# Kernel optimization log

Hardware: AMD Instinct MI355X
Metric: run time of the kernel (lower is better)

Reference implementation:

```python
import jax, jax.numpy as jnp
import numpy as np

B, L, H, N, CIN, COUT, U = 32, 12, 12, 2048, 2, 1, 64
K3 = 3  # num_matrices = n_supports * max_diffusion_step + 1 = 1*2 + 1


def setup_inputs() -> dict:
    rng = np.random.default_rng(0)
    # random sparse-ish symmetric adjacency -> scaled laplacian support (lambda_max ~= 2)
    A = rng.random((N, N), dtype=np.float32)
    A = np.maximum(A, A.T)
    A = A * (A > 0.995)
    d = A.sum(axis=1)
    dis = 1.0 / np.sqrt(np.maximum(d, 1e-6))
    Lap = np.eye(N, dtype=np.float32) - (dis[:, None] * A) * dis[None, :]
    support = (Lap - np.eye(N, dtype=np.float32)).astype(np.float32)  # 2/lmax*L - I with lmax=2

    key = jax.random.key(0)
    ks = jax.random.split(key, 6)

    def w(k, shape, fan):
        return jax.random.normal(k, shape, jnp.float32) / np.float32(np.sqrt(fan))

    Cg_e = (CIN + U) * K3   # 198
    Cg_d = (COUT + U) * K3  # 195
    return {
        "history_data": jax.random.normal(ks[0], (B, L, N, CIN), jnp.float32),
        "support": jnp.asarray(support),
        "enc_Wg": w(ks[1], (Cg_e, 2 * U), Cg_e),
        "enc_bg": jnp.ones((2 * U,), jnp.float32),  # gate bias starts at 1.0 (original repo)
        "enc_Wc": w(ks[2], (Cg_e, U), Cg_e),
        "enc_bc": jnp.zeros((U,), jnp.float32),
        "dec_Wg": w(ks[3], (Cg_d, 2 * U), Cg_d),
        "dec_bg": jnp.ones((2 * U,), jnp.float32),
        "dec_Wc": w(ks[4], (Cg_d, U), Cg_d),
        "dec_bc": jnp.zeros((U,), jnp.float32),
        "Wp": w(ks[5], (U, COUT), U),
        "bp": jnp.zeros((COUT,), jnp.float32),
    }


def _gconv(support, x, W, b):
    # x: [B, N, C]; Chebyshev diffusion T0=x, T1=Sx, T2=2S(Sx)-x, stacked feature-major
    x1 = jnp.einsum('mn,bnc->bmc', support, x)
    x2 = 2.0 * jnp.einsum('mn,bnc->bmc', support, x1) - x
    xs = jnp.stack([x, x1, x2], axis=-1)  # [B, N, C, 3]
    b_, n_, c_, k_ = xs.shape
    y = xs.reshape(b_ * n_, c_ * k_) @ W + b
    return y.reshape(b_, n_, -1)


def _cell(support, x, h, Wg, bg, Wc, bc):
    # DCGRU cell: x [B,N,in], h [B,N,U]
    cat = jnp.concatenate([x, h], axis=-1)
    ru = jax.nn.sigmoid(_gconv(support, cat, Wg, bg))
    r, u = jnp.split(ru, 2, axis=-1)
    c = jnp.tanh(_gconv(support, jnp.concatenate([x, r * h], axis=-1), Wc, bc))
    return u * h + (1.0 - u) * c


def reference(history_data, support, enc_Wg, enc_bg, enc_Wc, enc_bc,
              dec_Wg, dec_bg, dec_Wc, dec_bc, Wp, bp):
    hist = jnp.transpose(history_data, (1, 0, 2, 3))  # [L, B, N, CIN]
    h0 = jnp.zeros((B, N, U), history_data.dtype)

    def enc_step(h, xt):
        return _cell(support, xt, h, enc_Wg, enc_bg, enc_Wc, enc_bc), None

    h_enc, _ = jax.lax.scan(enc_step, h0, hist)

    go = jnp.zeros((B, N, COUT), history_data.dtype)

    def dec_step(carry, _):
        h, xin = carry
        h = _cell(support, xin, h, dec_Wg, dec_bg, dec_Wc, dec_bc)
        out = (h.reshape(-1, U) @ Wp + bp).reshape(B, N, COUT)
        return (h, out), out

    _, outs = jax.lax.scan(dec_step, (h_enc, go), None, length=H)  # [H, B, N, COUT]
    return jnp.transpose(outs, (1, 0, 2, 3))  # [B, H, N, COUT]
```

## Files before the change

kernel.cpp:

```cpp
#include <hip/hip_runtime.h>
#include <math.h>

#define NN 2048
#define BB 32
#define LL 12
#define HHH 12
#define UU 64
#define STR 68
#define SLAB (BB*STR)
#define SEGS 8
#define SEGW (SLAB/SEGS)
#define MR (NN*BB)
#define CSR_CAP 262144
#define PACK_HALF 28672

typedef short bfrag __attribute__((ext_vector_type(8)));
typedef float ffrag __attribute__((ext_vector_type(4)));

__device__ __forceinline__ unsigned packsf(float x) {
  unsigned u = __float_as_uint(x);
  unsigned hb = (u + 0x7FFFu + ((u >> 16) & 1u)) & 0xFFFF0000u;
  float rem = x - __uint_as_float(hb);
  unsigned lb = __float_as_uint(rem) >> 16;
  return hb | lb;
}
__device__ __forceinline__ float recsf(unsigned u) {
  return __uint_as_float(u & 0xFFFF0000u) + __uint_as_float(u << 16);
}
__device__ __forceinline__ float sigm(float x) { return 1.0f / (1.0f + __expf(-x)); }
__device__ __forceinline__ float tanhfast(float x) {
  float e = __expf(2.0f * x);
  return 1.0f - 2.0f / (e + 1.0f);
}

__global__ __launch_bounds__(256) void k_row_count(const float* __restrict__ S, int* __restrict__ cnt) {
  int m = blockIdx.x;
  const float* row = S + (size_t)m * NN;
  int c = 0;
  for (int i = threadIdx.x; i < NN; i += 256) c += (row[i] != 0.0f);
  __shared__ int sm[4];
  for (int off = 32; off; off >>= 1) c += __shfl_down(c, off, 64);
  if ((threadIdx.x & 63) == 0) sm[threadIdx.x >> 6] = c;
  __syncthreads();
  if (threadIdx.x == 0) cnt[m] = sm[0] + sm[1] + sm[2] + sm[3];
}

__global__ __launch_bounds__(256) void k_scan(const int* __restrict__ cnt, int* __restrict__ rp) {
  __shared__ int tot[256];
  int t = threadIdx.x;
  int base = t * 8;
  int v[8]; int s = 0;
  #pragma unroll
  for (int k = 0; k < 8; ++k) { v[k] = cnt[base + k]; s += v[k]; }
  tot[t] = s;
  __syncthreads();
  for (int off = 1; off < 256; off <<= 1) {
    int add = (t >= off) ? tot[t - off] : 0;
    __syncthreads();
    tot[t] += add;
    __syncthreads();
  }
  int run = (t == 0) ? 0 : tot[t - 1];
  #pragma unroll
  for (int k = 0; k < 8; ++k) { rp[base + k] = run; run += v[k]; }
  if (t == 255) rp[NN] = run;
}

__global__ __launch_bounds__(256) void k_fill(const float* __restrict__ S, const int* __restrict__ rp,
                                              int* __restrict__ cols, float* __restrict__ vals) {
  int m = blockIdx.x;
  const float* row = S + (size_t)m * NN;
  __shared__ int wsum[4];
  __shared__ int chunkbase;
  if (threadIdx.x == 0) chunkbase = rp[m];
  __syncthreads();
  int lane = threadIdx.x & 63, w = threadIdx.x >> 6;
  for (int ch = 0; ch < NN / 256; ++ch) {
    int i = ch * 256 + threadIdx.x;
    float val = row[i];
    bool p = (val != 0.0f);
    unsigned long long mask = __ballot(p);
    int rank = __popcll(mask & ((1ull << lane) - 1ull));
    if (lane == 0) wsum[w] = __popcll(mask);
    __syncthreads();
    int off = 0;
    for (int q = 0; q < w; ++q) off += wsum[q];
    if (p) { int k = chunkbase + off + rank; cols[k] = i; vals[k] = val; }
    __syncthreads();
    if (threadIdx.x == 0) chunkbase += wsum[0] + wsum[1] + wsum[2] + wsum[3];
    __syncthreads();
  }
}

__global__ __launch_bounds__(256) void k_pack(const float* __restrict__ Wsrc, unsigned short* __restrict__ dst,
                                              int CIN_, int NO) {
  int idx = blockIdx.x * 256 + threadIdx.x;
  int nh_count = NO >> 6;
  int tot = nh_count * 7 * 4 * 64 * 8;
  if (idx >= tot) return;
  int j = idx & 7;
  int r1 = idx >> 3;  int lane = r1 & 63;
  int r2 = r1 >> 6;   int nf = r2 & 3;
  int r3 = r2 >> 2;   int ks = r3 % 7; int nh = r3 / 7;
  int grp = lane >> 4, l15 = lane & 15;
  int col = nh*64 + nf*16 + l15;
  float wv = 0.0f;
  int kb = -1, c = 0;
  if (ks < 6) {
    kb = ks >> 1;
    c = CIN_ + (ks & 1)*32 + grp*8 + j;
  } else {
    int q = grp*8 + j;
    if (q < 3*CIN_) { kb = q / CIN_; c = q % CIN_; }
  }
  if (kb >= 0) {
    float w0 = Wsrc[((size_t)c*3 + 0)*NO + col];
    float w1 = Wsrc[((size_t)c*3 + 1)*NO + col];
    float w2 = Wsrc[((size_t)c*3 + 2)*NO + col];
    wv = (kb == 0) ? (w0 - w2) : ((kb == 1) ? w1 : 2.0f*w2);
  }
  unsigned pw = packsf(wv);
  size_t basehi = ((size_t)nh*PACK_HALF) + ((((size_t)ks*4 + nf)*2 + 0)*64 + lane)*8 + j;
  size_t baselo = ((size_t)nh*PACK_HALF) + ((((size_t)ks*4 + nf)*2 + 1)*64 + lane)*8 + j;
  dst[basehi] = (unsigned short)(pw >> 16);
  dst[baselo] = (unsigned short)(pw & 0xFFFFu);
}

__global__ __launch_bounds__(256) void k_packt(const float* __restrict__ src, unsigned* __restrict__ dst, int n) {
  int i = blockIdx.x * 256 + threadIdx.x;
  if (i < n) dst[i] = packsf(src[i]);
}

template<int SRC>
__global__ __launch_bounds__(256, 4) void k_hop(
    const int* __restrict__ rp, const int* __restrict__ cols, const float* __restrict__ vals,
    const unsigned* __restrict__ src, const unsigned* __restrict__ xP,
    const unsigned* __restrict__ hP, unsigned* __restrict__ Y, int t) {
  __shared__ int   scol[64];
  __shared__ float sval[64];
  int orig = blockIdx.x;
  int swz = (orig & 7) * 2048 + (orig >> 3);
  int seg = swz >> 11;
  int node = swz & 2047;
  int j0 = rp[node], j1 = rp[node + 1];
  int tid = threadIdx.x;
  int w0 = seg * SEGW + tid;
  bool a1 = tid < (SEGW - 256);
  int w1 = w0 + 256;
  float acc0 = 0.f, acc1 = 0.f;

  const unsigned *bp0, *bp1;
  unsigned st0, st1;
  bool z0 = false, z1 = false;
  if constexpr (SRC == 0) {
    bp0 = src + w0; st0 = SLAB;
    bp1 = src + (a1 ? w1 : w0); st1 = SLAB; z1 = !a1;
  } else {
    auto mk = [&](int wq, const unsigned*& bp, unsigned& st, bool& zz) {
      int b = wq / STR, c = wq - b * STR;
      if (c < 64) { bp = hP + (size_t)b * UU + c; st = BB * UU; }
      else if (SRC == 1 && c < 66) { bp = xP + ((size_t)(b * LL + t)) * NN * 2 + (c - 64); st = 2; }
      else if (SRC == 2 && c == 64) { bp = xP + b; st = BB; }
      else { bp = hP; st = 0; zz = true; }
    };
    mk(w0, bp0, st0, z0);
    if (a1) mk(w1, bp1, st1, z1);
    else { bp1 = hP; st1 = 0; z1 = true; }
  }

  for (int base = j0; base < j1; base += 64) {
    int cnt = min(64, j1 - base);
    if (tid < cnt) { scol[tid] = cols[base + tid]; sval[tid] = vals[base + tid]; }
    __syncthreads();
    int jj = 0;
    for (; jj + 8 <= cnt; jj += 8) {
      unsigned u0[8], u1[8];
      float sv[8];
      #pragma unroll
      for (int q = 0; q < 8; ++q) {
        unsigned n = (unsigned)scol[jj + q];
        sv[q] = sval[jj + q];
        u0[q] = bp0[(size_t)(n * st0)];
        u1[q] = bp1[(size_t)(n * st1)];
      }
      #pragma unroll
      for (int q = 0; q < 8; ++q) {
        acc0 = fmaf(sv[q], recsf(z0 ? 0u : u0[q]), acc0);
        acc1 = fmaf(sv[q], recsf(z1 ? 0u : u1[q]), acc1);
      }
    }
    for (; jj < cnt; ++jj) {
      unsigned n = (unsigned)scol[jj]; float s = sval[jj];
      unsigned a = bp0[(size_t)(n * st0)];
      unsigned b = bp1[(size_t)(n * st1)];
      acc0 = fmaf(s, recsf(z0 ? 0u : a), acc0);
      acc1 = fmaf(s, recsf(z1 ? 0u : b), acc1);
    }
    __syncthreads();
  }
  unsigned* yr = Y + (size_t)node * SLAB;
  yr[w0] = packsf(acc0);
  if (a1) yr[w1] = packsf(acc1);
}

template<int CATM>
__global__ __launch_bounds__(256, 4) void k_gate(
    const unsigned* __restrict__ hP, const unsigned* __restrict__ xP,
    const unsigned* __restrict__ T1P, const unsigned* __restrict__ T2P,
    const unsigned short* __restrict__ Bpack, const float* __restrict__ bg,
    unsigned* __restrict__ zP, float* __restrict__ Ug, int t) {
  int tid = threadIdx.x;
  int r0 = blockIdx.x * 64;
  int w = tid >> 6, lane = tid & 63, grp = lane >> 4, l15 = lane & 15;
  int row0 = r0 + w*16 + l15;
  ffrag acc[8];
  #pragma unroll
  for (int nf = 0; nf < 8; ++nf) acc[nf] = (ffrag){0.f, 0.f, 0.f, 0.f};

  #pragma unroll
  for (int ks = 0; ks < 7; ++ks) {
    int ko = (ks & 1)*32 + grp*8;
    bfrag ah0, al0;
    if (ks < 6) {
      const unsigned* p0; int st;
      if (ks < 2)      { p0 = hP;  st = UU; }
      else if (ks < 4) { p0 = T1P; st = STR; }
      else             { p0 = T2P; st = STR; }
      const unsigned* a0 = p0 + (size_t)row0*st + ko;
      uint4 q00 = *(const uint4*)a0, q01 = *(const uint4*)(a0 + 4);
      unsigned ua0[8] = {q00.x,q00.y,q00.z,q00.w,q01.x,q01.y,q01.z,q01.w};
      #pragma unroll
      for (int jj = 0; jj < 8; ++jj) {
        ah0[jj] = (short)(ua0[jj] >> 16); al0[jj] = (short)(ua0[jj] & 0xFFFFu);
      }
    } else {
      unsigned ua0[8] = {0,0,0,0,0,0,0,0};
      if (grp == 0) {
        if (CATM == 1) {
          int n0r = row0 >> 5, b0r = row0 & 31;
          const unsigned* hx0 = xP + (((size_t)(b0r*LL + t))*NN + n0r)*2;
          ua0[0] = hx0[0]; ua0[1] = hx0[1];
          ua0[2] = T1P[(size_t)row0*STR + 64]; ua0[3] = T1P[(size_t)row0*STR + 65];
          ua0[4] = T2P[(size_t)row0*STR + 64]; ua0[5] = T2P[(size_t)row0*STR + 65];
        } else {
          ua0[0] = xP[row0];
          ua0[1] = T1P[(size_t)row0*STR + 64];
          ua0[2] = T2P[(size_t)row0*STR + 64];
        }
      }
      #pragma unroll
      for (int jj = 0; jj < 8; ++jj) {
        ah0[jj] = (short)(ua0[jj] >> 16); al0[jj] = (short)(ua0[jj] & 0xFFFFu);
      }
    }
    #pragma unroll
    for (int nf = 0; nf < 8; ++nf) {
      const unsigned short* bb = Bpack + (size_t)(nf >> 2)*PACK_HALF
                               + (((size_t)(ks*4 + (nf & 3))*2)*64 + lane)*8;
      bfrag bh = *(const bfrag*)bb;
      bfrag bl = *(const bfrag*)(bb + 512);
      acc[nf] = __builtin_amdgcn_mfma_f32_16x16x32_bf16(ah0, bh, acc[nf], 0, 0, 0);
      acc[nf] = __builtin_amdgcn_mfma_f32_16x16x32_bf16(ah0, bl, acc[nf], 0, 0, 0);
      acc[nf] = __builtin_amdgcn_mfma_f32_16x16x32_bf16(al0, bh, acc[nf], 0, 0, 0);
    }
  }
  float bgv[8];
  #pragma unroll
  for (int nf = 0; nf < 8; ++nf) bgv[nf] = bg[nf*16 + l15];
  #pragma unroll
  for (int reg = 0; reg < 4; ++reg) {
    int row = r0 + w*16 + grp*4 + reg;
    #pragma unroll
    for (int nf = 0; nf < 8; ++nf) {
      int col = nf*16 + l15;
      float v = sigm(acc[nf][reg] + bgv[nf]);
      if (col < 64) {
        float ho = recsf(hP[(size_t)row*UU + col]);
        zP[(size_t)row*STR + col] = packsf(v * ho);
      } else {
        Ug[(size_t)row*UU + (col - 64)] = v;
      }
    }
  }
  if (l15 == 0) {
    #pragma unroll
    for (int reg = 0; reg < 4; ++reg) {
      int row = r0 + w*16 + grp*4 + reg;
      size_t zb = (size_t)row*STR;
      if (CATM == 1) {
        int n = row >> 5, b = row & 31;
        const unsigned* hx = xP + (((size_t)(b*LL + t))*NN + n)*2;
        zP[zb + 64] = hx[0]; zP[zb + 65] = hx[1];
      } else {
        zP[zb + 64] = xP[row]; zP[zb + 65] = 0u;
      }
      zP[zb + 66] = 0u; zP[zb + 67] = 0u;
    }
  }
}

template<bool DEC>
__global__ __launch_bounds__(256, 4) void k_cand(
    const unsigned* __restrict__ zP, const unsigned* __restrict__ T1P,
    const unsigned* __restrict__ T2P,
    const unsigned short* __restrict__ Bpack, const float* __restrict__ bc,
    const float* __restrict__ Ug, const unsigned* __restrict__ hOld,
    unsigned* __restrict__ hNew,
    const float* __restrict__ Wp, const float* __restrict__ bp,
    float* __restrict__ out, unsigned* __restrict__ xioP, int t) {
  int tid = threadIdx.x;
  int r0 = blockIdx.x * 64;
  int w = tid >> 6, lane = tid & 63, grp = lane >> 4, l15 = lane & 15;
  int row0 = r0 + w*16 + l15;
  ffrag acc[4];
  #pragma unroll
  for (int nf = 0; nf < 4; ++nf) acc[nf] = (ffrag){0.f, 0.f, 0.f, 0.f};

  #pragma unroll
  for (int ks = 0; ks < 7; ++ks) {
    int ko = (ks & 1)*32 + grp*8;
    bfrag ah0, al0;
    if (ks < 6) {
      const unsigned* p0;
      if (ks < 2)      p0 = zP;
      else if (ks < 4) p0 = T1P;
      else             p0 = T2P;
      const unsigned* a0 = p0 + (size_t)row0*STR + ko;
      uint4 q00 = *(const uint4*)a0, q01 = *(const uint4*)(a0 + 4);
      unsigned ua0[8] = {q00.x,q00.y,q00.z,q00.w,q01.x,q01.y,q01.z,q01.w};
      #pragma unroll
      for (int jj = 0; jj < 8; ++jj) {
        ah0[jj] = (short)(ua0[jj] >> 16); al0[jj] = (short)(ua0[jj] & 0xFFFFu);
      }
    } else {
      unsigned ua0[8] = {0,0,0,0,0,0,0,0};
      if (grp == 0) {
        if (!DEC) {
          ua0[0] = zP[(size_t)row0*STR + 64];  ua0[1] = zP[(size_t)row0*STR + 65];
          ua0[2] = T1P[(size_t)row0*STR + 64]; ua0[3] = T1P[(size_t)row0*STR + 65];
          ua0[4] = T2P[(size_t)row0*STR + 64]; ua0[5] = T2P[(size_t)row0*STR + 65];
        } else {
          ua0[0] = zP[(size_t)row0*STR + 64];
          ua0[1] = T1P[(size_t)row0*STR + 64];
          ua0[2] = T2P[(size_t)row0*STR + 64];
        }
      }
      #pragma unroll
      for (int jj = 0; jj < 8; ++jj) {
        ah0[jj] = (short)(ua0[jj] >> 16); al0[jj] = (short)(ua0[jj] & 0xFFFFu);
      }
    }
    #pragma unroll
    for (int nf = 0; nf < 4; ++nf) {
      const unsigned short* bb = Bpack + (((size_t)(ks*4 + nf)*2)*64 + lane)*8;
      bfrag bh = *(const bfrag*)bb;
      bfrag bl = *(const bfrag*)(bb + 512);
      acc[nf] = __builtin_amdgcn_mfma_f32_16x16x32_bf16(ah0, bh, acc[nf], 0, 0, 0);
      acc[nf] = __builtin_amdgcn_mfma_f32_16x16x32_bf16(ah0, bl, acc[nf], 0, 0, 0);
      acc[nf] = __builtin_amdgcn_mfma_f32_16x16x32_bf16(al0, bh, acc[nf], 0, 0, 0);
    }
  }
  float bcv[4], wpv[4];
  #pragma unroll
  for (int nf = 0; nf < 4; ++nf) {
    bcv[nf] = bc[nf*16 + l15];
    wpv[nf] = DEC ? Wp[nf*16 + l15] : 0.f;
  }
  float bp0 = DEC ? bp[0] : 0.f;
  #pragma unroll
  for (int reg = 0; reg < 4; ++reg) {
    int row = r0 + w*16 + grp*4 + reg;
    float p = 0.f;
    #pragma unroll
    for (int nf = 0; nf < 4; ++nf) {
      int col = nf*16 + l15;
      float cf = tanhfast(acc[nf][reg] + bcv[nf]);
      float u  = Ug[(size_t)row*UU + col];
      float ho = recsf(hOld[(size_t)row*UU + col]);
      float hv = u * ho + (1.0f - u) * cf;
      hNew[(size_t)row*UU + col] = packsf(hv);
      if (DEC) p = fmaf(hv, wpv[nf], p);
    }
    if (DEC) {
      p += __shfl_xor(p, 1, 64);
      p += __shfl_xor(p, 2, 64);
      p += __shfl_xor(p, 4, 64);
      p += __shfl_xor(p, 8, 64);
      if (l15 == 0) {
        float val = p + bp0;
        int n = row >> 5, b = row & 31;
        out[((size_t)b*HHH + t)*NN + n] = val;
        xioP[row] = packsf(val);
      }
    }
  }
}

extern "C" void kernel_launch(void* const* d_in, const int* in_sizes, int n_in,
                              void* d_out, int out_size, void* d_ws, size_t ws_size,
                              hipStream_t stream) {
  (void)in_sizes; (void)n_in; (void)out_size; (void)ws_size;
  const float* hist = (const float*)d_in[0];
  const float* support = (const float*)d_in[1];
  const float* eWg = (const float*)d_in[2];
  const float* ebg = (const float*)d_in[3];
  const float* eWc = (const float*)d_in[4];
  const float* ebc = (const float*)d_in[5];
  const float* dWg = (const float*)d_in[6];
  const float* dbg = (const float*)d_in[7];
  const float* dWc = (const float*)d_in[8];
  const float* dbc = (const float*)d_in[9];
  const float* Wp  = (const float*)d_in[10];
  const float* bp  = (const float*)d_in[11];
  float* out = (float*)d_out;

  char* base = (char*)d_ws;
  size_t off = 0;
  auto carve = [&](size_t bytes) -> void* {
    void* p = base + off;
    off += (bytes + 255) & ~(size_t)255;
    return p;
  };
  int*   cnt   = (int*)carve(NN * 4);
  int*   rpB   = (int*)carve((NN + 1) * 4);
  int*   colsB = (int*)carve(CSR_CAP * 4);
  float* valsB = (float*)carve(CSR_CAP * 4);
  unsigned short* Pge = (unsigned short*)carve(2 * PACK_HALF * 2);
  unsigned short* Pgd = (unsigned short*)carve(2 * PACK_HALF * 2);
  unsigned short* Pce = (unsigned short*)carve((size_t)PACK_HALF * 2);
  unsigned short* Pcd = (unsigned short*)carve((size_t)PACK_HALF * 2);
  unsigned* histP = (unsigned*)carve((size_t)BB * LL * NN * 2 * 4);
  unsigned* T1P   = (unsigned*)carve((size_t)NN * SLAB * 4);
  unsigned* T2P   = (unsigned*)carve((size_t)NN * SLAB * 4);
  unsigned* zP    = (unsigned*)carve((size_t)NN * SLAB * 4);
  float*    UgF   = (float*)carve((size_t)MR * UU * 4);
  unsigned* hPa   = (unsigned*)carve((size_t)MR * UU * 4);
  unsigned* hPb   = (unsigned*)carve((size_t)MR * UU * 4);
  unsigned* xioP  = (unsigned*)carve((size_t)MR * 4);

  hipMemsetAsync(hPa, 0, (size_t)MR * UU * 4, stream);
  hipMemsetAsync(xioP, 0, (size_t)MR * 4, stream);

  k_row_count<<<NN, 256, 0, stream>>>(support, cnt);
  k_scan<<<1, 256, 0, stream>>>(cnt, rpB);
  k_fill<<<NN, 256, 0, stream>>>(support, rpB, colsB, valsB);
  k_pack<<<112, 256, 0, stream>>>(eWg, Pge, 2, 128);
  k_pack<<<56, 256, 0, stream>>>(eWc, Pce, 2, 64);
  k_pack<<<112, 256, 0, stream>>>(dWg, Pgd, 1, 128);
  k_pack<<<56, 256, 0, stream>>>(dWc, Pcd, 1, 64);
  k_packt<<<(BB*LL*NN*2 + 255)/256, 256, 0, stream>>>(hist, histP, BB*LL*NN*2);

  unsigned* hc = hPa; unsigned* hn = hPb;
  for (int t = 0; t < LL; ++t) {
    k_hop<1><<<NN*SEGS, 256, 0, stream>>>(rpB, colsB, valsB, nullptr, histP, hc, T1P, t);
    k_hop<0><<<NN*SEGS, 256, 0, stream>>>(rpB, colsB, valsB, T1P, nullptr, nullptr, T2P, t);
    k_gate<1><<<MR/64, 256, 0, stream>>>(hc, histP, T1P, T2P, Pge, ebg, zP, UgF, t);
    k_hop<0><<<NN*SEGS, 256, 0, stream>>>(rpB, colsB, valsB, zP, nullptr, nullptr, T1P, t);
    k_hop<0><<<NN*SEGS, 256, 0, stream>>>(rpB, colsB, valsB, T1P, nullptr, nullptr, T2P, t);
    k_cand<false><<<MR/64, 256, 0, stream>>>(zP, T1P, T2P, Pce, ebc, UgF, hc, hn,
                                             Wp, bp, out, xioP, t);
    unsigned* tmp = hc; hc = hn; hn = tmp;
  }
  for (int t = 0; t < HHH; ++t) {
    k_hop<2><<<NN*SEGS, 256, 0, stream>>>(rpB, colsB, valsB, nullptr, xioP, hc, T1P, t);
    k_hop<0><<<NN*SEGS, 256, 0, stream>>>(rpB, colsB, valsB, T1P, nullptr, nullptr, T2P, t);
    k_gate<2><<<MR/64, 256, 0, stream>>>(hc, xioP, T1P, T2P, Pgd, dbg, zP, UgF, t);
    k_hop<0><<<NN*SEGS, 256, 0, stream>>>(rpB, colsB, valsB, zP, nullptr, nullptr, T1P, t);
    k_hop<0><<<NN*SEGS, 256, 0, stream>>>(rpB, colsB, valsB, T1P, nullptr, nullptr, T2P, t);
    k_cand<true><<<MR/64, 256, 0, stream>>>(zP, T1P, T2P, Pcd, dbc, UgF, hc, hn,
                                            Wp, bp, out, xioP, t);
    unsigned* tmp = hc; hc = hn; hn = tmp;
  }
}
```

Before: 4.588 ms.

## Store activations as fp32 in padded concat slabs and split to bf16 in GEMM

Intermediate buffers change from packed hi/lo bf16 words to plain fp32, with the hidden state kept in the same padded [N,B,68] slab layout that the hop kernels read. The hop kernel becomes one column per thread with 320 threads, no shared-memory staging, and CSR column offsets premultiplied by the slab stride. The bf16 hi/lo split moves into the MFMA operand load of the gate and candidate kernels. This removes the per-gather unpack and repack work and the special-case source addressing for x and h, and a small k_setx kernel now writes the input features each step. The cost is fp32 gathers of the same width, fp32 cat buffers, and an extra launch per encoder step.

```diff
diff --git a/kernel.cpp b/kernel.cpp
--- a/kernel.cpp
+++ b/kernel.cpp
@@ -17,20 +17,24 @@
 typedef short bfrag __attribute__((ext_vector_type(8)));
 typedef float ffrag __attribute__((ext_vector_type(4)));
 
-__device__ __forceinline__ unsigned packsf(float x) {
-  unsigned u = __float_as_uint(x);
-  unsigned hb = (u + 0x7FFFu + ((u >> 16) & 1u)) & 0xFFFF0000u;
-  float rem = x - __uint_as_float(hb);
-  unsigned lb = __float_as_uint(rem) >> 16;
-  return hb | lb;
-}
-__device__ __forceinline__ float recsf(unsigned u) {
-  return __uint_as_float(u & 0xFFFF0000u) + __uint_as_float(u << 16);
-}
 __device__ __forceinline__ float sigm(float x) { return 1.0f / (1.0f + __expf(-x)); }
 __device__ __forceinline__ float tanhfast(float x) {
   float e = __expf(2.0f * x);
   return 1.0f - 2.0f / (e + 1.0f);
+}
+
+__device__ __forceinline__ void cvt8(const float* a, bfrag* hi, bfrag* lo) {
+  bfrag H, L;
+  #pragma unroll
+  for (int j = 0; j < 8; ++j) {
+    unsigned u = __float_as_uint(a[j]);
+    unsigned hb = (u + 0x7FFFu + ((u >> 16) & 1u)) >> 16;
+    float rem = a[j] - __uint_as_float(hb << 16);
+    unsigned u2 = __float_as_uint(rem);
+    unsigned lb = (u2 + 0x7FFFu + ((u2 >> 16) & 1u)) >> 16;
+    H[j] = (short)hb; L[j] = (short)lb;
+  }
+  *hi = H; *lo = L;
 }
 
 __global__ __launch_bounds__(256) void k_row_count(const float* __restrict__ S, int* __restrict__ cnt) {
@@ -85,7 +89,7 @@
     __syncthreads();
     int off = 0;
     for (int q = 0; q < w; ++q) off += wsum[q];
-    if (p) { int k = chunkbase + off + rank; cols[k] = i; vals[k] = val; }
+    if (p) { int k = chunkbase + off + rank; cols[k] = i * SLAB; vals[k] = val; }
     __syncthreads();
     if (threadIdx.x == 0) chunkbase += wsum[0] + wsum[1] + wsum[2] + wsum[3];
     __syncthreads();
@@ -119,96 +123,59 @@
     float w2 = Wsrc[((size_t)c*3 + 2)*NO + col];
     wv = (kb == 0) ? (w0 - w2) : ((kb == 1) ? w1 : 2.0f*w2);
   }
-  unsigned pw = packsf(wv);
+  unsigned u = __float_as_uint(wv);
+  unsigned hb = (u + 0x7FFFu + ((u >> 16) & 1u)) >> 16;
+  float rem = wv - __uint_as_float(hb << 16);
+  unsigned u2 = __float_as_uint(rem);
+  unsigned lb = (u2 + 0x7FFFu + ((u2 >> 16) & 1u)) >> 16;
   size_t basehi = ((size_t)nh*PACK_HALF) + ((((size_t)ks*4 + nf)*2 + 0)*64 + lane)*8 + j;
   size_t baselo = ((size_t)nh*PACK_HALF) + ((((size_t)ks*4 + nf)*2 + 1)*64 + lane)*8 + j;
-  dst[basehi] = (unsigned short)(pw >> 16);
-  dst[baselo] = (unsigned short)(pw & 0xFFFFu);
-}
-
-__global__ __launch_bounds__(256) void k_packt(const float* __restrict__ src, unsigned* __restrict__ dst, int n) {
-  int i = blockIdx.x * 256 + threadIdx.x;
-  if (i < n) dst[i] = packsf(src[i]);
-}
-
-template<int SRC>
-__global__ __launch_bounds__(256, 4) void k_hop(
-    const int* __restrict__ rp, const int* __restrict__ cols, const float* __restrict__ vals,
-    const unsigned* __restrict__ src, const unsigned* __restrict__ xP,
-    const unsigned* __restrict__ hP, unsigned* __restrict__ Y, int t) {
-  __shared__ int   scol[64];
-  __shared__ float sval[64];
+  dst[basehi] = (unsigned short)hb;
+  dst[baselo] = (unsigned short)lb;
+}
+
+__global__ __launch_bounds__(256) void k_setx(const float* __restrict__ hist, float* __restrict__ cat, int t) {
+  int idx = blockIdx.x * 256 + threadIdx.x;
+  if (idx >= MR * 2) return;
+  int c = idx & 1, row = idx >> 1;
+  int n = row >> 5, b = row & 31;
+  cat[(size_t)row * STR + 64 + c] = hist[(((size_t)(b * LL + t)) * NN + n) * 2 + c];
+}
+
+__global__ __launch_bounds__(320) void k_hop(
+    const int* __restrict__ rp, const int* __restrict__ colsS, const float* __restrict__ vals,
+    const float* __restrict__ src, float* __restrict__ Y) {
   int orig = blockIdx.x;
   int swz = (orig & 7) * 2048 + (orig >> 3);
   int seg = swz >> 11;
   int node = swz & 2047;
+  int tid = threadIdx.x;
+  if (tid >= SEGW) return;
+  int w0 = seg * SEGW + tid;
   int j0 = rp[node], j1 = rp[node + 1];
-  int tid = threadIdx.x;
-  int w0 = seg * SEGW + tid;
-  bool a1 = tid < (SEGW - 256);
-  int w1 = w0 + 256;
   float acc0 = 0.f, acc1 = 0.f;
-
-  const unsigned *bp0, *bp1;
-  unsigned st0, st1;
-  bool z0 = false, z1 = false;
-  if constexpr (SRC == 0) {
-    bp0 = src + w0; st0 = SLAB;
-    bp1 = src + (a1 ? w1 : w0); st1 = SLAB; z1 = !a1;
-  } else {
-    auto mk = [&](int wq, const unsigned*& bp, unsigned& st, bool& zz) {
-      int b = wq / STR, c = wq - b * STR;
-      if (c < 64) { bp = hP + (size_t)b * UU + c; st = BB * UU; }
-      else if (SRC == 1 && c < 66) { bp = xP + ((size_t)(b * LL + t)) * NN * 2 + (c - 64); st = 2; }
-      else if (SRC == 2 && c == 64) { bp = xP + b; st = BB; }
-      else { bp = hP; st = 0; zz = true; }
-    };
-    mk(w0, bp0, st0, z0);
-    if (a1) mk(w1, bp1, st1, z1);
-    else { bp1 = hP; st1 = 0; z1 = true; }
-  }
-
-  for (int base = j0; base < j1; base += 64) {
-    int cnt = min(64, j1 - base);
-    if (tid < cnt) { scol[tid] = cols[base + tid]; sval[tid] = vals[base + tid]; }
-    __syncthreads();
-    int jj = 0;
-    for (; jj + 8 <= cnt; jj += 8) {
-      unsigned u0[8], u1[8];
-      float sv[8];
-      #pragma unroll
-      for (int q = 0; q < 8; ++q) {
-        unsigned n = (unsigned)scol[jj + q];
-        sv[q] = sval[jj + q];
-        u0[q] = bp0[(size_t)(n * st0)];
-        u1[q] = bp1[(size_t)(n * st1)];
-      }
-      #pragma unroll
-      for (int q = 0; q < 8; ++q) {
-        acc0 = fmaf(sv[q], recsf(z0 ? 0u : u0[q]), acc0);
-        acc1 = fmaf(sv[q], recsf(z1 ? 0u : u1[q]), acc1);
-      }
-    }
-    for (; jj < cnt; ++jj) {
-      unsigned n = (unsigned)scol[jj]; float s = sval[jj];
-      unsigned a = bp0[(size_t)(n * st0)];
-      unsigned b = bp1[(size_t)(n * st1)];
-      acc0 = fmaf(s, recsf(z0 ? 0u : a), acc0);
-      acc1 = fmaf(s, recsf(z1 ? 0u : b), acc1);
-    }
-    __syncthreads();
-  }
-  unsigned* yr = Y + (size_t)node * SLAB;
-  yr[w0] = packsf(acc0);
-  if (a1) yr[w1] = packsf(acc1);
+  int j = j0;
+  for (; j + 4 <= j1; j += 4) {
+    int   o0 = colsS[j],   o1 = colsS[j+1], o2 = colsS[j+2], o3 = colsS[j+3];
+    float s0 = vals[j],    s1 = vals[j+1],  s2 = vals[j+2],  s3 = vals[j+3];
+    float v0 = src[o0 + w0];
+    float v1 = src[o1 + w0];
+    float v2 = src[o2 + w0];
+    float v3 = src[o3 + w0];
+    acc0 = fmaf(s0, v0, acc0);
+    acc1 = fmaf(s1, v1, acc1);
+    acc0 = fmaf(s2, v2, acc0);
+    acc1 = fmaf(s3, v3, acc1);
+  }
+  for (; j < j1; ++j) acc0 = fmaf(vals[j], src[colsS[j] + w0], acc0);
+  Y[(size_t)node * SLAB + w0] = acc0 + acc1;
 }
 
 template<int CATM>
 __global__ __launch_bounds__(256, 4) void k_gate(
-    const unsigned* __restrict__ hP, const unsigned* __restrict__ xP,
-    const unsigned* __restrict__ T1P, const unsigned* __restrict__ T2P,
+    const float* __restrict__ catP, const float* __restrict__ T1P, const float* __restrict__ T2P,
     const unsigned short* __restrict__ Bpack, const float* __restrict__ bg,
-    unsigned* __restrict__ zP, float* __restrict__ Ug, int t) {
+    float* __restrict__ zP, float* __restrict__ Ug) {
   int tid = threadIdx.x;
   int r0 = blockIdx.x * 64;
   int w = tid >> 6, lane = tid & 63, grp = lane >> 4, l15 = lane & 15;
@@ -220,39 +187,26 @@
   #pragma unroll
   for (int ks = 0; ks < 7; ++ks) {
     int ko = (ks & 1)*32 + grp*8;
+    float av[8] = {0,0,0,0,0,0,0,0};
+    if (ks < 6) {
+      const float* p0 = (ks < 2) ? catP : ((ks < 4) ? T1P : T2P);
+      const float* a0 = p0 + (size_t)row0*STR + ko;
+      *(float4*)(av)     = *(const float4*)a0;
+      *(float4*)(av + 4) = *(const float4*)(a0 + 4);
+    } else if (grp == 0) {
+      size_t rb = (size_t)row0*STR + 64;
+      if (CATM == 1) {
+        av[0] = catP[rb];  av[1] = catP[rb + 1];
+        av[2] = T1P[rb];   av[3] = T1P[rb + 1];
+        av[4] = T2P[rb];   av[5] = T2P[rb + 1];
+      } else {
+        av[0] = catP[rb];
+        av[1] = T1P[rb];
+        av[2] = T2P[rb];
+      }
+    }
     bfrag ah0, al0;
-    if (ks < 6) {
-      const unsigned* p0; int st;
-      if (ks < 2)      { p0 = hP;  st = UU; }
-      else if (ks < 4) { p0 = T1P; st = STR; }
-      else             { p0 = T2P; st = STR; }
-      const unsigned* a0 = p0 + (size_t)row0*st + ko;
-      uint4 q00 = *(const uint4*)a0, q01 = *(const uint4*)(a0 + 4);
-      unsigned ua0[8] = {q00.x,q00.y,q00.z,q00.w,q01.x,q01.y,q01.z,q01.w};
-      #pragma unroll
-      for (int jj = 0; jj < 8; ++jj) {
-        ah0[jj] = (short)(ua0[jj] >> 16); al0[jj] = (short)(ua0[jj] & 0xFFFFu);
-      }
-    } else {
-      unsigned ua0[8] = {0,0,0,0,0,0,0,0};
-      if (grp == 0) {
-        if (CATM == 1) {
-          int n0r = row0 >> 5, b0r = row0 & 31;
-          const unsigned* hx0 = xP + (((size_t)(b0r*LL + t))*NN + n0r)*2;
-          ua0[0] = hx0[0]; ua0[1] = hx0[1];
-          ua0[2] = T1P[(size_t)row0*STR + 64]; ua0[3] = T1P[(size_t)row0*STR + 65];
-          ua0[4] = T2P[(size_t)row0*STR + 64]; ua0[5] = T2P[(size_t)row0*STR + 65];
-        } else {
-          ua0[0] = xP[row0];
-          ua0[1] = T1P[(size_t)row0*STR + 64];
-          ua0[2] = T2P[(size_t)row0*STR + 64];
-        }
-      }
-      #pragma unroll
-      for (int jj = 0; jj < 8; ++jj) {
-        ah0[jj] = (short)(ua0[jj] >> 16); al0[jj] = (short)(ua0[jj] & 0xFFFFu);
-      }
-    }
+    cvt8(av, &ah0, &al0);
     #pragma unroll
     for (int nf = 0; nf < 8; ++nf) {
       const unsigned short* bb = Bpack + (size_t)(nf >> 2)*PACK_HALF
@@ -275,8 +229,8 @@
       int col = nf*16 + l15;
       float v = sigm(acc[nf][reg] + bgv[nf]);
       if (col < 64) {
-        float ho = recsf(hP[(size_t)row*UU + col]);
-        zP[(size_t)row*STR + col] = packsf(v * ho);
+        float ho = catP[(size_t)row*STR + col];
+        zP[(size_t)row*STR + col] = v * ho;
       } else {
         Ug[(size_t)row*UU + (col - 64)] = v;
       }
@@ -287,27 +241,21 @@
     for (int reg = 0; reg < 4; ++reg) {
       int row = r0 + w*16 + grp*4 + reg;
       size_t zb = (size_t)row*STR;
-      if (CATM == 1) {
-        int n = row >> 5, b = row & 31;
-        const unsigned* hx = xP + (((size_t)(b*LL + t))*NN + n)*2;
-        zP[zb + 64] = hx[0]; zP[zb + 65] = hx[1];
-      } else {
-        zP[zb + 64] = xP[row]; zP[zb + 65] = 0u;
-      }
-      zP[zb + 66] = 0u; zP[zb + 67] = 0u;
+      zP[zb + 64] = catP[zb + 64];
+      zP[zb + 65] = (CATM == 1) ? catP[zb + 65] : 0.f;
+      zP[zb + 66] = 0.f; zP[zb + 67] = 0.f;
     }
   }
 }
 
 template<bool DEC>
 __global__ __launch_bounds__(256, 4) void k_cand(
-    const unsigned* __restrict__ zP, const unsigned* __restrict__ T1P,
-    const unsigned* __restrict__ T2P,
+    const float* __restrict__ zP, const float* __restrict__ T1P, const float* __restrict__ T2P,
     const unsigned short* __restrict__ Bpack, const float* __restrict__ bc,
-    const float* __restrict__ Ug, const unsigned* __restrict__ hOld,
-    unsigned* __restrict__ hNew,
+    const float* __restrict__ Ug, const float* __restrict__ catCur,
+    float* __restrict__ catNext,
     const float* __restrict__ Wp, const float* __restrict__ bp,
-    float* __restrict__ out, unsigned* __restrict__ xioP, int t) {
+    float* __restrict__ out, int t) {
   int tid = threadIdx.x;
   int r0 = blockIdx.x * 64;
   int w = tid >> 6, lane = tid & 63, grp = lane >> 4, l15 = lane & 15;
@@ -319,37 +267,26 @@
   #pragma unroll
   for (int ks = 0; ks < 7; ++ks) {
     int ko = (ks & 1)*32 + grp*8;
+    float av[8] = {0,0,0,0,0,0,0,0};
+    if (ks < 6) {
+      const float* p0 = (ks < 2) ? zP : ((ks < 4) ? T1P : T2P);
+      const float* a0 = p0 + (size_t)row0*STR + ko;
+      *(float4*)(av)     = *(const float4*)a0;
+      *(float4*)(av + 4) = *(const float4*)(a0 + 4);
+    } else if (grp == 0) {
+      size_t rb = (size_t)row0*STR + 64;
+      if (!DEC) {
+        av[0] = zP[rb];  av[1] = zP[rb + 1];
+        av[2] = T1P[rb]; av[3] = T1P[rb + 1];
+        av[4] = T2P[rb]; av[5] = T2P[rb + 1];
+      } else {
+        av[0] = zP[rb];
+        av[1] = T1P[rb];
+        av[2] = T2P[rb];
+      }
+    }
     bfrag ah0, al0;
-    if (ks < 6) {
-      const unsigned* p0;
-      if (ks < 2)      p0 = zP;
-      else if (ks < 4) p0 = T1P;
-      else             p0 = T2P;
-      const unsigned* a0 = p0 + (size_t)row0*STR + ko;
-      uint4 q00 = *(const uint4*)a0, q01 = *(const uint4*)(a0 + 4);
-      unsigned ua0[8] = {q00.x,q00.y,q00.z,q00.w,q01.x,q01.y,q01.z,q01.w};
-      #pragma unroll
-      for (int jj = 0; jj < 8; ++jj) {
-        ah0[jj] = (short)(ua0[jj] >> 16); al0[jj] = (short)(ua0[jj] & 0xFFFFu);
-      }
-    } else {
-      unsigned ua0[8] = {0,0,0,0,0,0,0,0};
-      if (grp == 0) {
-        if (!DEC) {
-          ua0[0] = zP[(size_t)row0*STR + 64];  ua0[1] = zP[(size_t)row0*STR + 65];
-          ua0[2] = T1P[(size_t)row0*STR + 64]; ua0[3] = T1P[(size_t)row0*STR + 65];
-          ua0[4] = T2P[(size_t)row0*STR + 64]; ua0[5] = T2P[(size_t)row0*STR + 65];
-        } else {
-          ua0[0] = zP[(size_t)row0*STR + 64];
-          ua0[1] = T1P[(size_t)row0*STR + 64];
-          ua0[2] = T2P[(size_t)row0*STR + 64];
-        }
-      }
-      #pragma unroll
-      for (int jj = 0; jj < 8; ++jj) {
-        ah0[jj] = (short)(ua0[jj] >> 16); al0[jj] = (short)(ua0[jj] & 0xFFFFu);
-      }
-    }
+    cvt8(av, &ah0, &al0);
     #pragma unroll
     for (int nf = 0; nf < 4; ++nf) {
       const unsigned short* bb = Bpack + (((size_t)(ks*4 + nf)*2)*64 + lane)*8;
@@ -376,9 +313,9 @@
       int col = nf*16 + l15;
       float cf = tanhfast(acc[nf][reg] + bcv[nf]);
       float u  = Ug[(size_t)row*UU + col];
-      float ho = recsf(hOld[(size_t)row*UU + col]);
+      float ho = catCur[(size_t)row*STR + col];
       float hv = u * ho + (1.0f - u) * cf;
-      hNew[(size_t)row*UU + col] = packsf(hv);
+      catNext[(size_t)row*STR + col] = hv;
       if (DEC) p = fmaf(hv, wpv[nf], p);
     }
     if (DEC) {
@@ -390,7 +327,13 @@
         float val = p + bp0;
         int n = row >> 5, b = row & 31;
         out[((size_t)b*HHH + t)*NN + n] = val;
-        xioP[row] = packsf(val);
+        catNext[(size_t)row*STR + 64] = val;
+        catNext[(size_t)row*STR + 65] = 0.f;
+      }
+    } else {
+      if (l15 == 0) {
+        catNext[(size_t)row*STR + 64] = 0.f;
+        catNext[(size_t)row*STR + 65] = 0.f;
       }
     }
   }
@@ -429,17 +372,15 @@
   unsigned short* Pgd = (unsigned short*)carve(2 * PACK_HALF * 2);
   unsigned short* Pce = (unsigned short*)carve((size_t)PACK_HALF * 2);
   unsigned short* Pcd = (unsigned short*)carve((size_t)PACK_HALF * 2);
-  unsigned* histP = (unsigned*)carve((size_t)BB * LL * NN * 2 * 4);
-  unsigned* T1P   = (unsigned*)carve((size_t)NN * SLAB * 4);
-  unsigned* T2P   = (unsigned*)carve((size_t)NN * SLAB * 4);
-  unsigned* zP    = (unsigned*)carve((size_t)NN * SLAB * 4);
-  float*    UgF   = (float*)carve((size_t)MR * UU * 4);
-  unsigned* hPa   = (unsigned*)carve((size_t)MR * UU * 4);
-  unsigned* hPb   = (unsigned*)carve((size_t)MR * UU * 4);
-  unsigned* xioP  = (unsigned*)carve((size_t)MR * 4);
-
-  hipMemsetAsync(hPa, 0, (size_t)MR * UU * 4, stream);
-  hipMemsetAsync(xioP, 0, (size_t)MR * 4, stream);
+  float* T1P  = (float*)carve((size_t)NN * SLAB * 4);
+  float* T2P  = (float*)carve((size_t)NN * SLAB * 4);
+  float* zP   = (float*)carve((size_t)NN * SLAB * 4);
+  float* UgF  = (float*)carve((size_t)MR * UU * 4);
+  float* catA = (float*)carve((size_t)NN * SLAB * 4);
+  float* catB = (float*)carve((size_t)NN * SLAB * 4);
+
+  hipMemsetAsync(catA, 0, (size_t)NN * SLAB * 4, stream);
+  hipMemsetAsync(catB, 0, (size_t)NN * SLAB * 4, stream);
 
   k_row_count<<<NN, 256, 0, stream>>>(support, cnt);
   k_scan<<<1, 256, 0, stream>>>(cnt, rpB);
@@ -448,27 +389,27 @@
   k_pack<<<56, 256, 0, stream>>>(eWc, Pce, 2, 64);
   k_pack<<<112, 256, 0, stream>>>(dWg, Pgd, 1, 128);
   k_pack<<<56, 256, 0, stream>>>(dWc, Pcd, 1, 64);
-  k_packt<<<(BB*LL*NN*2 + 255)/256, 256, 0, stream>>>(hist, histP, BB*LL*NN*2);
-
-  unsigned* hc = hPa; unsigned* hn = hPb;
+
+  float* hc = catA; float* hn = catB;
   for (int t = 0; t < LL; ++t) {
-    k_hop<1><<<NN*SEGS, 256, 0, stream>>>(rpB, colsB, valsB, nullptr, histP, hc, T1P, t);
-    k_hop<0><<<NN*SEGS, 256, 0, stream>>>(rpB, colsB, valsB, T1P, nullptr, nullptr, T2P, t);
-    k_gate<1><<<MR/64, 256, 0, stream>>>(hc, histP, T1P, T2P, Pge, ebg, zP, UgF, t);
-    k_hop<0><<<NN*SEGS, 256, 0, stream>>>(rpB, colsB, valsB, zP, nullptr, nullptr, T1P, t);
-    k_hop<0><<<NN*SEGS, 256, 0, stream>>>(rpB, colsB, valsB, T1P, nullptr, nullptr, T2P, t);
+    k_setx<<<(MR*2 + 255)/256, 256, 0, stream>>>(hist, hc, t);
+    k_hop<<<NN*SEGS, 320, 0, stream>>>(rpB, colsB, valsB, hc, T1P);
+    k_hop<<<NN*SEGS, 320, 0, stream>>>(rpB, colsB, valsB, T1P, T2P);
+    k_gate<1><<<MR/64, 256, 0, stream>>>(hc, T1P, T2P, Pge, ebg, zP, UgF);
+    k_hop<<<NN*SEGS, 320, 0, stream>>>(rpB, colsB, valsB, zP, T1P);
+    k_hop<<<NN*SEGS, 320, 0, stream>>>(rpB, colsB, valsB, T1P, T2P);
     k_cand<false><<<MR/64, 256, 0, stream>>>(zP, T1P, T2P, Pce, ebc, UgF, hc, hn,
-                                             Wp, bp, out, xioP, t);
-    unsigned* tmp = hc; hc = hn; hn = tmp;
+                                             Wp, bp, out, t);
+    float* tmp = hc; hc = hn; hn = tmp;
   }
   for (int t = 0; t < HHH; ++t) {
-    k_hop<2><<<NN*SEGS, 256, 0, stream>>>(rpB, colsB, valsB, nullptr, xioP, hc, T1P, t);
-    k_hop<0><<<NN*SEGS, 256, 0, stream>>>(rpB, colsB, valsB, T1P, nullptr, nullptr, T2P, t);
-    k_gate<2><<<MR/64, 256, 0, stream>>>(hc, xioP, T1P, T2P, Pgd, dbg, zP, UgF, t);
-    k_hop<0><<<NN*SEGS, 256, 0, stream>>>(rpB, colsB, valsB, zP, nullptr, nullptr, T1P, t);
-    k_hop<0><<<NN*SEGS, 256, 0, stream>>>(rpB, colsB, valsB, T1P, nullptr, nullptr, T2P, t);
+    k_hop<<<NN*SEGS, 320, 0, stream>>>(rpB, colsB, valsB, hc, T1P);
+    k_hop<<<NN*SEGS, 320, 0, stream>>>(rpB, colsB, valsB, T1P, T2P);
+    k_gate<2><<<MR/64, 256, 0, stream>>>(hc, T1P, T2P, Pgd, dbg, zP, UgF);
+    k_hop<<<NN*SEGS, 320, 0, stream>>>(rpB, colsB, valsB, zP, T1P);
+    k_hop<<<NN*SEGS, 320, 0, stream>>>(rpB, colsB, valsB, T1P, T2P);
     k_cand<true><<<MR/64, 256, 0, stream>>>(zP, T1P, T2P, Pcd, dbc, UgF, hc, hn,
-                                            Wp, bp, out, xioP, t);
-    unsigned* tmp = hc; hc = hn; hn = tmp;
-  }
-}
+                                            Wp, bp, out, t);
+    float* tmp = hc; hc = hn; hn = tmp;
+  }
+}
```

Measured after the change: 4.489 ms. 2.2% less time.
